# Performance work log

Hardware: AMD Instinct MI355X
Metric: run time of the kernel (lower is better)

The kernel has to match this reference:

```python
import jax, jax.numpy as jnp
import numpy as np

N, E, IN, HID, OUT = 50000, 1600000, 64, 32, 32
NEG_SLOPE = 0.2  # PyG GATConv default


def gat_conv(x, src, dst, W, a_src, a_dst, b, n):
    """Single-head PyG-style GATConv (dropout off / eval mode).
    x: [n, in], src/dst: [E+n] (self-loops already appended),
    W: [in, out], a_src/a_dst: [out], b: [out]."""
    h = x @ W                                   # [n, out]
    e_src = (h * a_src).sum(-1)                 # [n]
    e_dst = (h * a_dst).sum(-1)                 # [n]
    alpha = jax.nn.leaky_relu(e_src[src] + e_dst[dst], NEG_SLOPE)  # [Etot]
    amax = jax.ops.segment_max(alpha, dst, num_segments=n)         # per-dst max
    ex = jnp.exp(alpha - amax[dst])
    denom = jax.ops.segment_sum(ex, dst, num_segments=n)
    coef = ex / denom[dst]                      # softmax over incoming edges
    out = jax.ops.segment_sum(h[src] * coef[:, None], dst, num_segments=n)
    return out + b


def branch(x, src, dst, W1, as1, ad1, b1, W2, as2, ad2, b2, lW, lb, n):
    h = jax.nn.relu(gat_conv(x, src, dst, W1, as1, ad1, b1, n))
    h = jax.nn.relu(gat_conv(h, src, dst, W2, as2, ad2, b2, n))
    return h @ lW + lb


def setup_inputs() -> dict:
    key = jax.random.key(0)
    ks = jax.random.split(key, 32)
    inp = {
        "x": jax.random.normal(ks[0], (N, IN), dtype=jnp.float32),
        "edge_index": jax.random.randint(ks[1], (2, E), 0, N, dtype=jnp.int64),
    }
    i = 2
    for p in ("c", "r"):
        dims = [(IN, HID), (HID, HID)]
        for li, (di, do) in enumerate(dims, start=1):
            s = (2.0 / (di + do)) ** 0.5
            inp[f"{p}_W{li}"] = jax.random.normal(ks[i], (di, do), dtype=jnp.float32) * s; i += 1
            inp[f"{p}_as{li}"] = jax.random.normal(ks[i], (do,), dtype=jnp.float32) * 0.1; i += 1
            inp[f"{p}_ad{li}"] = jax.random.normal(ks[i], (do,), dtype=jnp.float32) * 0.1; i += 1
            inp[f"{p}_b{li}"] = jnp.zeros((do,), dtype=jnp.float32); i += 1
        inp[f"{p}_lW"] = jax.random.normal(ks[i], (HID, OUT), dtype=jnp.float32) * (2.0 / (HID + OUT)) ** 0.5; i += 1
        inp[f"{p}_lb"] = jnp.zeros((OUT,), dtype=jnp.float32); i += 1
    return inp


def reference(x, edge_index,
              c_W1, c_as1, c_ad1, c_b1, c_W2, c_as2, c_ad2, c_b2, c_lW, c_lb,
              r_W1, r_as1, r_ad1, r_b1, r_W2, r_as2, r_ad2, r_b2, r_lW, r_lb):
    n = x.shape[0]
    loop = jnp.arange(n, dtype=edge_index.dtype)
    src = jnp.concatenate([edge_index[0], loop])  # add_self_loops=True default
    dst = jnp.concatenate([edge_index[1], loop])
    prob_zero = jax.nn.sigmoid(branch(x, src, dst, c_W1, c_as1, c_ad1, c_b1,
                                      c_W2, c_as2, c_ad2, c_b2, c_lW, c_lb, n))
    res = branch(x, src, dst, r_W1, r_as1, r_ad1, r_b1,
                 r_W2, r_as2, r_ad2, r_b2, r_lW, r_lb, n)
    return (prob_zero, res)
```

## Files before the change

### kernel.cpp

```cpp
#include <hip/hip_runtime.h>
#include <hip/hip_fp16.h>
#include <math.h>

#define NEG_SLOPE 0.2f

#define DSHIFT 7
#define DSZ 128
#define NBUCK_MAX 512
#define PART_BLOCKS 256

typedef __attribute__((ext_vector_type(8))) _Float16 v8h;
typedef __attribute__((ext_vector_type(4))) float v4f;
typedef __attribute__((ext_vector_type(4))) unsigned int v4u;

__device__ __forceinline__ int ntload_i(const int* p) {
    return __builtin_nontemporal_load(p);
}

__global__ __launch_bounds__(256)
void xcast_kernel(const float* __restrict__ x, _Float16* __restrict__ xh,
                  int total4, int* __restrict__ bcount) {
    int i = blockIdx.x * blockDim.x + threadIdx.x;
    if (i < NBUCK_MAX) bcount[i] = 0;
    if (i >= total4) return;
    float4 v = ((const float4*)x)[i];
    _Float16 o[4] = {(_Float16)v.x, (_Float16)v.y, (_Float16)v.z, (_Float16)v.w};
    ((uint2*)xh)[i] = *(const uint2*)o;
}

__global__ __launch_bounds__(256)
void part_count_kernel(const int* __restrict__ ei, int E, int n, int nbuck,
                       int* __restrict__ bcount) {
    __shared__ int cnt[NBUCK_MAX];
    int t = threadIdx.x;
    for (int k = t; k < nbuck; k += 256) cnt[k] = 0;
    __syncthreads();
    int Etot = E + n;
    int chunk = (Etot + gridDim.x - 1) / gridDim.x;
    int s0 = blockIdx.x * chunk;
    int s1 = min(Etot, s0 + chunk);
    for (int i = s0 + t; i < s1; i += 256) {
        int d = (i < E) ? ntload_i(ei + E + i) : (i - E);
        if ((unsigned)d < (unsigned)n) atomicAdd(&cnt[d >> DSHIFT], 1);
    }
    __syncthreads();
    for (int k = t; k < nbuck; k += 256) {
        int c = cnt[k];
        if (c) atomicAdd(&bcount[k], c);
    }
}

__global__ void bucket_scan_kernel(const int* __restrict__ bcount,
                                   int* __restrict__ colbase,
                                   int* __restrict__ pcur,
                                   int* __restrict__ rptr,
                                   int n, int nbuck) {
    __shared__ int sm[512];
    int t = threadIdx.x;
    int v = (t < nbuck) ? bcount[t] : 0;
    sm[t] = v;
    __syncthreads();
    int x = v;
    for (int off = 1; off < 512; off <<= 1) {
        int y = (t >= off) ? sm[t - off] : 0;
        __syncthreads();
        x += y;
        sm[t] = x;
        __syncthreads();
    }
    if (t < nbuck) { colbase[t] = x - v; pcur[t] = x - v; }
    if (t == nbuck - 1) rptr[n] = x;
}

__global__ __launch_bounds__(256)
void part_write_kernel(const int* __restrict__ ei, int E, int n, int nbuck,
                       int* __restrict__ pcur,
                       unsigned* __restrict__ pairs) {
    __shared__ int cnt[NBUCK_MAX];
    __shared__ int lcur[NBUCK_MAX];
    int t = threadIdx.x;
    for (int k = t; k < nbuck; k += 256) cnt[k] = 0;
    __syncthreads();
    int Etot = E + n;
    int chunk = (Etot + gridDim.x - 1) / gridDim.x;
    int s0 = blockIdx.x * chunk;
    int s1 = min(Etot, s0 + chunk);
    for (int i = s0 + t; i < s1; i += 256) {
        int d = (i < E) ? ntload_i(ei + E + i) : (i - E);
        if ((unsigned)d < (unsigned)n) atomicAdd(&cnt[d >> DSHIFT], 1);
    }
    __syncthreads();
    for (int k = t; k < nbuck; k += 256) {
        int c = cnt[k];
        if (c) lcur[k] = atomicAdd(&pcur[k], c);
    }
    __syncthreads();
    for (int i = s0 + t; i < s1; i += 256) {
        int s, d;
        if (i < E) { s = ntload_i(ei + i); d = ntload_i(ei + E + i); }
        else       { s = d = i - E; }
        if ((unsigned)d < (unsigned)n) {
            if ((unsigned)s >= (unsigned)n) s = 0;
            int pos = atomicAdd(&lcur[d >> DSHIFT], 1);
            pairs[pos] = (unsigned)s | ((unsigned)(d & (DSZ - 1)) << 16);
        }
    }
}

__global__ __launch_bounds__(256)
void fine_kernel(const unsigned* __restrict__ pairs,
                 const int* __restrict__ colbase,
                 const int* __restrict__ bcount,
                 int* __restrict__ rptr,
                 int* __restrict__ col, int n) {
    __shared__ int cnt[DSZ];
    __shared__ int ofs[DSZ];
    int b = blockIdx.x, t = threadIdx.x;
    int p0 = colbase[b], p1 = p0 + bcount[b];
    if (t < DSZ) cnt[t] = 0;
    __syncthreads();
    for (int i = p0 + t; i < p1; i += 256)
        atomicAdd(&cnt[pairs[i] >> 16], 1);
    __syncthreads();
    int v = (t < DSZ) ? cnt[t] : 0;
    if (t < DSZ) ofs[t] = v;
    __syncthreads();
    int x = v;
    for (int off = 1; off < DSZ; off <<= 1) {
        int y = (t >= off && t < DSZ) ? ofs[t - off] : 0;
        __syncthreads();
        if (t < DSZ) { x += y; ofs[t] = x; }
        __syncthreads();
    }
    int d0 = b << DSHIFT;
    if (t < DSZ) {
        int start = p0 + x - v;
        if (d0 + t < n) rptr[d0 + t] = start;
        cnt[t] = start;
    }
    __syncthreads();
    for (int i = p0 + t; i < p1; i += 256) {
        unsigned u = pairs[i];
        int pos = atomicAdd(&cnt[u >> 16], 1);
        col[pos] = (int)(u & 0xFFFFu);
    }
}

__global__ void prep_kernel(const float* __restrict__ cW1, const float* __restrict__ rW1,
                            const float* __restrict__ cas1, const float* __restrict__ cad1,
                            const float* __restrict__ ras1, const float* __restrict__ rad1,
                            const float* __restrict__ cW2, const float* __restrict__ rW2,
                            const float* __restrict__ cas2, const float* __restrict__ cad2,
                            const float* __restrict__ ras2, const float* __restrict__ rad2,
                            const float* __restrict__ clW, const float* __restrict__ rlW,
                            _Float16* __restrict__ WB1,
                            _Float16* __restrict__ WB2,
                            _Float16* __restrict__ WBh) {
    __shared__ float f1s[2][64], f1d[2][64];
    __shared__ float f2s[2][32], f2d[2][32];
    int t = threadIdx.x;
    if (t < 128) {
        int b = t >> 6, k = t & 63;
        const float* W   = b ? rW1 : cW1;
        const float* as_ = b ? ras1 : cas1;
        const float* ad_ = b ? rad1 : cad1;
        float s1 = 0.f, s2 = 0.f;
        for (int f = 0; f < 32; ++f) {
            s1 = fmaf(W[k * 32 + f], as_[f], s1);
            s2 = fmaf(W[k * 32 + f], ad_[f], s2);
        }
        f1s[b][k] = s1;
        f1d[b][k] = s2;
    } else if (t < 192) {
        int b = (t - 128) >> 5, k = (t - 128) & 31;
        const float* W   = b ? rW2 : cW2;
        const float* as_ = b ? ras2 : cas2;
        const float* ad_ = b ? rad2 : cad2;
        float s1 = 0.f, s2 = 0.f;
        for (int f = 0; f < 32; ++f) {
            s1 = fmaf(W[k * 32 + f], as_[f], s1);
            s2 = fmaf(W[k * 32 + f], ad_[f], s2);
        }
        f2s[b][k] = s1;
        f2d[b][k] = s2;
    }
    __syncthreads();
    for (int idx = t; idx < 6144; idx += 256) {
        int blk = idx >> 9;
        int l = (idx >> 3) & 63, j = idx & 7;
        int b = blk / 6, rem = blk % 6, c = rem / 3, tt = rem % 3;
        int k = c * 32 + (l >> 4) * 8 + j;
        int nn = l & 15;
        const float* W = b ? rW1 : cW1;
        float v;
        if (tt < 2) v = W[k * 32 + tt * 16 + nn];
        else v = (nn == 0) ? f1s[b][k] : ((nn == 1) ? f1d[b][k] : 0.f);
        WB1[idx] = (_Float16)v;
    }
    for (int idx = t; idx < 3072; idx += 256) {
        int blk = idx >> 9;
        int l = (idx >> 3) & 63, j = idx & 7;
        int b = blk / 3, tt = blk % 3;
        int k = (l >> 4) * 8 + j;
        int nn = l & 15;
        const float* W = b ? rW2 : cW2;
        float v;
        if (tt < 2) v = W[k * 32 + tt * 16 + nn];
        else v = (nn == 0) ? f2s[b][k] : ((nn == 1) ? f2d[b][k] : 0.f);
        WB2[idx] = (_Float16)v;
    }
    for (int idx = t; idx < 2048; idx += 256) {
        int blk = idx >> 9;
        int l = (idx >> 3) & 63, j = idx & 7;
        int b = blk >> 1, tt = blk & 1;
        int k = (l >> 4) * 8 + j;
        int nn = l & 15;
        const float* W = b ? rlW : clW;
        WBh[idx] = (_Float16)W[k * 32 + tt * 16 + nn];
    }
}

__global__ __launch_bounds__(256)
void t1_mfma_kernel(const _Float16* __restrict__ xh,
                    const _Float16* __restrict__ WB1,
                    _Float16* __restrict__ hC, _Float16* __restrict__ hR,
                    float* __restrict__ esC, float* __restrict__ edC,
                    float* __restrict__ esR, float* __restrict__ edR, int n) {
    int wave = (blockIdx.x * blockDim.x + threadIdx.x) >> 6;
    int lane = threadIdx.x & 63;
    int ntiles = n >> 4;
    if (wave >= ntiles) return;
    int m0 = wave << 4;
    int quad = lane >> 4, nn = lane & 15;
    const _Float16* arow = xh + (size_t)(m0 + nn) * 64 + quad * 8;
    v8h a0 = *(const v8h*)arow;
    v8h a1 = *(const v8h*)(arow + 32);
    v4f acc[2][3];
#pragma unroll
    for (int b = 0; b < 2; ++b)
#pragma unroll
        for (int tt = 0; tt < 3; ++tt) acc[b][tt] = (v4f){0.f, 0.f, 0.f, 0.f};
#pragma unroll
    for (int b = 0; b < 2; ++b) {
#pragma unroll
        for (int c = 0; c < 2; ++c) {
            v8h av = c ? a1 : a0;
#pragma unroll
            for (int tt = 0; tt < 3; ++tt) {
                v8h wb = *(const v8h*)(WB1 + (((b * 2 + c) * 3 + tt) << 9) + lane * 8);
                acc[b][tt] = __builtin_amdgcn_mfma_f32_16x16x32_f16(av, wb, acc[b][tt], 0, 0, 0);
            }
        }
    }
#pragma unroll
    for (int i = 0; i < 4; ++i) {
        int m = m0 + quad * 4 + i;
        size_t r = (size_t)m * 32;
        hC[r + nn]      = (_Float16)acc[0][0][i];
        hC[r + 16 + nn] = (_Float16)acc[0][1][i];
        hR[r + nn]      = (_Float16)acc[1][0][i];
        hR[r + 16 + nn] = (_Float16)acc[1][1][i];
        if (nn == 0) { esC[m] = acc[0][2][i]; esR[m] = acc[1][2][i]; }
        if (nn == 1) { edC[m] = acc[0][2][i]; edR[m] = acc[1][2][i]; }
    }
}

__global__ __launch_bounds__(256)
void t2_mfma_kernel(const _Float16* __restrict__ gC,
                    const _Float16* __restrict__ gR,
                    const _Float16* __restrict__ WB2,
                    _Float16* __restrict__ hC, _Float16* __restrict__ hR,
                    float* __restrict__ esC, float* __restrict__ edC,
                    float* __restrict__ esR, float* __restrict__ edR, int n) {
    int wave = (blockIdx.x * blockDim.x + threadIdx.x) >> 6;
    int lane = threadIdx.x & 63;
    if (wave >= (n >> 4)) return;
    int m0 = wave << 4;
    int quad = lane >> 4, nn = lane & 15;
    v8h aC = *(const v8h*)(gC + (size_t)(m0 + nn) * 32 + quad * 8);
    v8h aR = *(const v8h*)(gR + (size_t)(m0 + nn) * 32 + quad * 8);
    v4f acc[2][3];
#pragma unroll
    for (int b = 0; b < 2; ++b)
#pragma unroll
        for (int tt = 0; tt < 3; ++tt) acc[b][tt] = (v4f){0.f, 0.f, 0.f, 0.f};
#pragma unroll
    for (int b = 0; b < 2; ++b) {
        v8h av = b ? aR : aC;
#pragma unroll
        for (int tt = 0; tt < 3; ++tt) {
            v8h wb = *(const v8h*)(WB2 + ((b * 3 + tt) << 9) + lane * 8);
            acc[b][tt] = __builtin_amdgcn_mfma_f32_16x16x32_f16(av, wb, acc[b][tt], 0, 0, 0);
        }
    }
#pragma unroll
    for (int i = 0; i < 4; ++i) {
        int m = m0 + quad * 4 + i;
        size_t r = (size_t)m * 32;
        hC[r + nn]      = (_Float16)acc[0][0][i];
        hC[r + 16 + nn] = (_Float16)acc[0][1][i];
        hR[r + nn]      = (_Float16)acc[1][0][i];
        hR[r + 16 + nn] = (_Float16)acc[1][1][i];
        if (nn == 0) { esC[m] = acc[0][2][i]; esR[m] = acc[1][2][i]; }
        if (nn == 1) { edC[m] = acc[0][2][i]; edR[m] = acc[1][2][i]; }
    }
}

__global__ __launch_bounds__(256)
void head_mfma_kernel(const _Float16* __restrict__ gC,
                      const _Float16* __restrict__ gR,
                      const _Float16* __restrict__ WBh,
                      const float* __restrict__ clb,
                      const float* __restrict__ rlb,
                      float* __restrict__ out, int n) {
    int wave = (blockIdx.x * blockDim.x + threadIdx.x) >> 6;
    int lane = threadIdx.x & 63;
    if (wave >= (n >> 4)) return;
    int m0 = wave << 4;
    int quad = lane >> 4, nn = lane & 15;
    v8h aC = *(const v8h*)(gC + (size_t)(m0 + nn) * 32 + quad * 8);
    v8h aR = *(const v8h*)(gR + (size_t)(m0 + nn) * 32 + quad * 8);
    v4f acc[2][2];
#pragma unroll
    for (int b = 0; b < 2; ++b)
#pragma unroll
        for (int tt = 0; tt < 2; ++tt) acc[b][tt] = (v4f){0.f, 0.f, 0.f, 0.f};
#pragma unroll
    for (int b = 0; b < 2; ++b) {
        v8h av = b ? aR : aC;
#pragma unroll
        for (int tt = 0; tt < 2; ++tt) {
            v8h wb = *(const v8h*)(WBh + ((b * 2 + tt) << 9) + lane * 8);
            acc[b][tt] = __builtin_amdgcn_mfma_f32_16x16x32_f16(av, wb, acc[b][tt], 0, 0, 0);
        }
    }
    float lb0c = clb[nn], lb1c = clb[16 + nn];
    float lb0r = rlb[nn], lb1r = rlb[16 + nn];
#pragma unroll
    for (int i = 0; i < 4; ++i) {
        int m = m0 + quad * 4 + i;
        float y0 = acc[0][0][i] + lb0c;
        float y1 = acc[0][1][i] + lb1c;
        out[(size_t)m * 32 + nn]      = 1.f / (1.f + __expf(-y0));
        out[(size_t)m * 32 + 16 + nn] = 1.f / (1.f + __expf(-y1));
        out[(size_t)n * 32 + (size_t)m * 32 + nn]      = acc[1][0][i] + lb0r;
        out[(size_t)n * 32 + (size_t)m * 32 + 16 + nn] = acc[1][1][i] + lb1r;
    }
}

__global__ __launch_bounds__(256, 8)
void agg_kernel(const int* __restrict__ rptr,
                const int* __restrict__ col,
                const _Float16* __restrict__ hp,
                const float* __restrict__ es,
                const float* __restrict__ ed,
                const float* __restrict__ bias,
                _Float16* __restrict__ gout, int n) {
    int grp = (blockIdx.x * blockDim.x + threadIdx.x) >> 5;
    int lane = threadIdx.x & 31;
    int sub = lane >> 2;
    int fq  = lane & 3;
    if (grp >= n) return;
    int d = grp;
    int beg = rptr[d], end = rptr[d + 1];
    float edv = ed[d];
    float acc[8];
#pragma unroll
    for (int i = 0; i < 8; ++i) acc[i] = 0.f;
    float l = 0.f;
#pragma unroll 2
    for (int base = beg; base + sub < end; base += 8) {
        int e = base + sub;
        int s = ntload_i(col + e);
        float t = es[s] + edv;
        t = (t > 0.f) ? t : NEG_SLOPE * t;
        float ex = __expf(t);
        l += ex;
        uint4 q = *(const uint4*)(hp + (size_t)s * 32 + fq * 8);
        const __half2* h2 = (const __half2*)&q;
#pragma unroll
        for (int i = 0; i < 4; ++i) {
            float2 v = __half22float2(h2[i]);
            acc[2 * i]     = fmaf(v.x, ex, acc[2 * i]);
            acc[2 * i + 1] = fmaf(v.y, ex, acc[2 * i + 1]);
        }
    }
#pragma unroll
    for (int off = 4; off <= 16; off <<= 1) {
        l += __shfl_xor(l, off, 32);
#pragma unroll
        for (int i = 0; i < 8; ++i) acc[i] += __shfl_xor(acc[i], off, 32);
    }
    if (sub == 0) {
        float il = 1.f / l;
        __half2 o[4];
#pragma unroll
        for (int j = 0; j < 4; ++j) {
            float g0 = fmaxf(acc[2 * j] * il + bias[fq * 8 + 2 * j], 0.f);
            float g1 = fmaxf(acc[2 * j + 1] * il + bias[fq * 8 + 2 * j + 1], 0.f);
            o[j] = __floats2half2_rn(g0, g1);
        }
        __builtin_nontemporal_store(*(const v4u*)o,
                                    (v4u*)(gout + (size_t)d * 32 + fq * 8));
    }
}

extern "C" void kernel_launch(void* const* d_in, const int* in_sizes, int n_in,
                              void* d_out, int out_size, void* d_ws, size_t ws_size,
                              hipStream_t stream) {
    const float* x = (const float*)d_in[0];
    const int* ei = (const int*)d_in[1];
    const int N = in_sizes[0] / 64;
    const int E = in_sizes[1] / 2;
    const int Etot = E + N;

    const float* cW1  = (const float*)d_in[2];
    const float* cas1 = (const float*)d_in[3];
    const float* cad1 = (const float*)d_in[4];
    const float* cb1  = (const float*)d_in[5];
    const float* cW2  = (const float*)d_in[6];
    const float* cas2 = (const float*)d_in[7];
    const float* cad2 = (const float*)d_in[8];
    const float* cb2  = (const float*)d_in[9];
    const float* clW  = (const float*)d_in[10];
    const float* clb  = (const float*)d_in[11];
    const float* rW1  = (const float*)d_in[12];
    const float* ras1 = (const float*)d_in[13];
    const float* rad1 = (const float*)d_in[14];
    const float* rb1  = (const float*)d_in[15];
    const float* rW2  = (const float*)d_in[16];
    const float* ras2 = (const float*)d_in[17];
    const float* rad2 = (const float*)d_in[18];
    const float* rb2  = (const float*)d_in[19];
    const float* rlW  = (const float*)d_in[20];
    const float* rlb  = (const float*)d_in[21];

    const int nbuck = (N + DSZ - 1) >> DSHIFT;

    char* w = (char*)d_ws;
    size_t off = 0;
    auto alloc = [&](size_t bytes) {
        void* p = w + off;
        off = (off + bytes + 255) & ~(size_t)255;
        return p;
    };
    int*       rptr    = (int*)alloc((size_t)(N + 1) * 4);
    int*       bcount  = (int*)alloc(NBUCK_MAX * 4);
    int*       colbase = (int*)alloc(NBUCK_MAX * 4);
    int*       pcur    = (int*)alloc(NBUCK_MAX * 4);
    int*       col     = (int*)alloc((size_t)Etot * 4);
    unsigned*  pairs   = (unsigned*)alloc((size_t)Etot * 4);
    _Float16*  hC      = (_Float16*)alloc((size_t)N * 32 * 2);
    _Float16*  hR      = (_Float16*)alloc((size_t)N * 32 * 2);
    _Float16*  gC      = (_Float16*)alloc((size_t)N * 32 * 2);
    _Float16*  gR      = (_Float16*)alloc((size_t)N * 32 * 2);
    float*     esAC    = (float*)alloc((size_t)N * 4);
    float*     edAC    = (float*)alloc((size_t)N * 4);
    float*     esAR    = (float*)alloc((size_t)N * 4);
    float*     edAR    = (float*)alloc((size_t)N * 4);
    float*     esBC    = (float*)alloc((size_t)N * 4);
    float*     edBC    = (float*)alloc((size_t)N * 4);
    float*     esBR    = (float*)alloc((size_t)N * 4);
    float*     edBR    = (float*)alloc((size_t)N * 4);
    _Float16*  xh      = (_Float16*)alloc((size_t)N * 64 * 2);
    _Float16*  WB1     = (_Float16*)alloc(6144 * 2);
    _Float16*  WB2     = (_Float16*)alloc(3072 * 2);
    _Float16*  WBh     = (_Float16*)alloc(2048 * 2);
    (void)ws_size;

    float* out = (float*)d_out;
    const int node_blocks = (N * 32 + 255) / 256;
    const int xc_blocks   = (N * 64 / 4 + 255) / 256;
    const int mfma_blocks = ((N >> 4) * 64 + 255) / 256;

    xcast_kernel<<<xc_blocks, 256, 0, stream>>>(x, xh, N * 64 / 4, bcount);
    prep_kernel<<<1, 256, 0, stream>>>(cW1, rW1, cas1, cad1, ras1, rad1,
                                       cW2, rW2, cas2, cad2, ras2, rad2,
                                       clW, rlW, WB1, WB2, WBh);
    part_count_kernel<<<PART_BLOCKS, 256, 0, stream>>>(ei, E, N, nbuck, bcount);
    bucket_scan_kernel<<<1, 512, 0, stream>>>(bcount, colbase, pcur, rptr, N, nbuck);
    part_write_kernel<<<PART_BLOCKS, 256, 0, stream>>>(ei, E, N, nbuck, pcur, pairs);
    fine_kernel<<<nbuck, 256, 0, stream>>>(pairs, colbase, bcount, rptr, col, N);

    t1_mfma_kernel<<<mfma_blocks, 256, 0, stream>>>(xh, WB1, hC, hR,
                                                    esAC, edAC, esAR, edAR, N);
    agg_kernel<<<node_blocks, 256, 0, stream>>>(
        rptr, col, hC, esAC, edAC, cb1, gC, N);
    agg_kernel<<<node_blocks, 256, 0, stream>>>(
        rptr, col, hR, esAR, edAR, rb1, gR, N);

    t2_mfma_kernel<<<mfma_blocks, 256, 0, stream>>>(gC, gR, WB2, hC, hR,
                                                    esBC, edBC, esBR, edBR, N);
    agg_kernel<<<node_blocks, 256, 0, stream>>>(
        rptr, col, hC, esBC, edBC, cb2, gC, N);
    agg_kernel<<<node_blocks, 256, 0, stream>>>(
        rptr, col, hR, esBR, edBR, rb2, gR, N);
    head_mfma_kernel<<<mfma_blocks, 256, 0, stream>>>(gC, gR, WBh, clb, rlb, out, N);
}
```

Baseline: 310.5 us.

## Fuse classifier and regressor aggregations and fold x cast into first GEMM

The two per-branch aggregation kernels of each layer are merged into one that walks the CSR neighbour list once and accumulates both branches. The attention scalars are stored interleaved as float2 so one gather serves both branches. The separate fp32→fp16 cast kernel for x is removed: t1 now reads fp32 x and converts in registers, and bucket-count zeroing moves into prep_kernel. This cuts duplicate col/index traffic and launches, at the cost of doubled register pressure in the aggregation kernel, which may lower occupancy.

```diff
diff --git a/kernel.cpp b/kernel.cpp
--- a/kernel.cpp
+++ b/kernel.cpp
@@ -11,21 +11,86 @@
 
 typedef __attribute__((ext_vector_type(8))) _Float16 v8h;
 typedef __attribute__((ext_vector_type(4))) float v4f;
-typedef __attribute__((ext_vector_type(4))) unsigned int v4u;
 
 __device__ __forceinline__ int ntload_i(const int* p) {
     return __builtin_nontemporal_load(p);
 }
 
-__global__ __launch_bounds__(256)
-void xcast_kernel(const float* __restrict__ x, _Float16* __restrict__ xh,
-                  int total4, int* __restrict__ bcount) {
-    int i = blockIdx.x * blockDim.x + threadIdx.x;
-    if (i < NBUCK_MAX) bcount[i] = 0;
-    if (i >= total4) return;
-    float4 v = ((const float4*)x)[i];
-    _Float16 o[4] = {(_Float16)v.x, (_Float16)v.y, (_Float16)v.z, (_Float16)v.w};
-    ((uint2*)xh)[i] = *(const uint2*)o;
+__global__ void prep_kernel(const float* __restrict__ cW1, const float* __restrict__ rW1,
+                            const float* __restrict__ cas1, const float* __restrict__ cad1,
+                            const float* __restrict__ ras1, const float* __restrict__ rad1,
+                            const float* __restrict__ cW2, const float* __restrict__ rW2,
+                            const float* __restrict__ cas2, const float* __restrict__ cad2,
+                            const float* __restrict__ ras2, const float* __restrict__ rad2,
+                            const float* __restrict__ clW, const float* __restrict__ rlW,
+                            _Float16* __restrict__ WB1,
+                            _Float16* __restrict__ WB2,
+                            _Float16* __restrict__ WBh,
+                            int* __restrict__ bcount) {
+    __shared__ float f1s[2][64], f1d[2][64];
+    __shared__ float f2s[2][32], f2d[2][32];
+    int t = threadIdx.x;
+    bcount[t] = 0;
+    bcount[t + 256] = 0;
+    if (t < 128) {
+        int b = t >> 6, k = t & 63;
+        const float* W   = b ? rW1 : cW1;
+        const float* as_ = b ? ras1 : cas1;
+        const float* ad_ = b ? rad1 : cad1;
+        float s1 = 0.f, s2 = 0.f;
+        for (int f = 0; f < 32; ++f) {
+            s1 = fmaf(W[k * 32 + f], as_[f], s1);
+            s2 = fmaf(W[k * 32 + f], ad_[f], s2);
+        }
+        f1s[b][k] = s1;
+        f1d[b][k] = s2;
+    } else if (t < 192) {
+        int b = (t - 128) >> 5, k = (t - 128) & 31;
+        const float* W   = b ? rW2 : cW2;
+        const float* as_ = b ? ras2 : cas2;
+        const float* ad_ = b ? rad2 : cad2;
+        float s1 = 0.f, s2 = 0.f;
+        for (int f = 0; f < 32; ++f) {
+            s1 = fmaf(W[k * 32 + f], as_[f], s1);
+            s2 = fmaf(W[k * 32 + f], ad_[f], s2);
+        }
+        f2s[b][k] = s1;
+        f2d[b][k] = s2;
+    }
+    __syncthreads();
+    for (int idx = t; idx < 6144; idx += 256) {
+        int blk = idx >> 9;
+        int l = (idx >> 3) & 63, j = idx & 7;
+        int b = blk / 6, rem = blk % 6, c = rem / 3, tt = rem % 3;
+        int k = c * 32 + (l >> 4) * 8 + j;
+        int nn = l & 15;
+        const float* W = b ? rW1 : cW1;
+        float v;
+        if (tt < 2) v = W[k * 32 + tt * 16 + nn];
+        else v = (nn == 0) ? f1s[b][k] : ((nn == 1) ? f1d[b][k] : 0.f);
+        WB1[idx] = (_Float16)v;
+    }
+    for (int idx = t; idx < 3072; idx += 256) {
+        int blk = idx >> 9;
+        int l = (idx >> 3) & 63, j = idx & 7;
+        int b = blk / 3, tt = blk % 3;
+        int k = (l >> 4) * 8 + j;
+        int nn = l & 15;
+        const float* W = b ? rW2 : cW2;
+        float v;
+        if (tt < 2) v = W[k * 32 + tt * 16 + nn];
+        else v = (nn == 0) ? f2s[b][k] : ((nn == 1) ? f2d[b][k] : 0.f);
+        WB2[idx] = (_Float16)v;
+    }
+    for (int idx = t; idx < 2048; idx += 256) {
+        int blk = idx >> 9;
+        int l = (idx >> 3) & 63, j = idx & 7;
+        int b = blk >> 1, tt = blk & 1;
+        int k = (l >> 4) * 8 + j;
+        int nn = l & 15;
+        const float* W = b ? rlW : clW;
+        WBh[idx] = (_Float16)W[k * 32 + tt * 16 + nn];
+    }
 }
 
 __global__ __launch_bounds__(256)
@@ -146,95 +211,31 @@
     }
 }
 
-__global__ void prep_kernel(const float* __restrict__ cW1, const float* __restrict__ rW1,
-                            const float* __restrict__ cas1, const float* __restrict__ cad1,
-                            const float* __restrict__ ras1, const float* __restrict__ rad1,
-                            const float* __restrict__ cW2, const float* __restrict__ rW2,
-                            const float* __restrict__ cas2, const float* __restrict__ cad2,
-                            const float* __restrict__ ras2, const float* __restrict__ rad2,
-                            const float* __restrict__ clW, const float* __restrict__ rlW,
-                            _Float16* __restrict__ WB1,
-                            _Float16* __restrict__ WB2,
-                            _Float16* __restrict__ WBh) {
-    __shared__ float f1s[2][64], f1d[2][64];
-    __shared__ float f2s[2][32], f2d[2][32];
-    int t = threadIdx.x;
-    if (t < 128) {
-        int b = t >> 6, k = t & 63;
-        const float* W   = b ? rW1 : cW1;
-        const float* as_ = b ? ras1 : cas1;
-        const float* ad_ = b ? rad1 : cad1;
-        float s1 = 0.f, s2 = 0.f;
-        for (int f = 0; f < 32; ++f) {
-            s1 = fmaf(W[k * 32 + f], as_[f], s1);
-            s2 = fmaf(W[k * 32 + f], ad_[f], s2);
-        }
-        f1s[b][k] = s1;
-        f1d[b][k] = s2;
-    } else if (t < 192) {
-        int b = (t - 128) >> 5, k = (t - 128) & 31;
-        const float* W   = b ? rW2 : cW2;
-        const float* as_ = b ? ras2 : cas2;
-        const float* ad_ = b ? rad2 : cad2;
-        float s1 = 0.f, s2 = 0.f;
-        for (int f = 0; f < 32; ++f) {
-            s1 = fmaf(W[k * 32 + f], as_[f], s1);
-            s2 = fmaf(W[k * 32 + f], ad_[f], s2);
-        }
-        f2s[b][k] = s1;
-        f2d[b][k] = s2;
-    }
-    __syncthreads();
-    for (int idx = t; idx < 6144; idx += 256) {
-        int blk = idx >> 9;
-        int l = (idx >> 3) & 63, j = idx & 7;
-        int b = blk / 6, rem = blk % 6, c = rem / 3, tt = rem % 3;
-        int k = c * 32 + (l >> 4) * 8 + j;
-        int nn = l & 15;
-        const float* W = b ? rW1 : cW1;
-        float v;
-        if (tt < 2) v = W[k * 32 + tt * 16 + nn];
-        else v = (nn == 0) ? f1s[b][k] : ((nn == 1) ? f1d[b][k] : 0.f);
-        WB1[idx] = (_Float16)v;
-    }
-    for (int idx = t; idx < 3072; idx += 256) {
-        int blk = idx >> 9;
-        int l = (idx >> 3) & 63, j = idx & 7;
-        int b = blk / 3, tt = blk % 3;
-        int k = (l >> 4) * 8 + j;
-        int nn = l & 15;
-        const float* W = b ? rW2 : cW2;
-        float v;
-        if (tt < 2) v = W[k * 32 + tt * 16 + nn];
-        else v = (nn == 0) ? f2s[b][k] : ((nn == 1) ? f2d[b][k] : 0.f);
-        WB2[idx] = (_Float16)v;
-    }
-    for (int idx = t; idx < 2048; idx += 256) {
-        int blk = idx >> 9;
-        int l = (idx >> 3) & 63, j = idx & 7;
-        int b = blk >> 1, tt = blk & 1;
-        int k = (l >> 4) * 8 + j;
-        int nn = l & 15;
-        const float* W = b ? rlW : clW;
-        WBh[idx] = (_Float16)W[k * 32 + tt * 16 + nn];
-    }
-}
-
 __global__ __launch_bounds__(256)
-void t1_mfma_kernel(const _Float16* __restrict__ xh,
+void t1_mfma_kernel(const float* __restrict__ x,
                     const _Float16* __restrict__ WB1,
                     _Float16* __restrict__ hC, _Float16* __restrict__ hR,
-                    float* __restrict__ esC, float* __restrict__ edC,
-                    float* __restrict__ esR, float* __restrict__ edR, int n) {
+                    float2* __restrict__ es2, float2* __restrict__ ed2, int n) {
     int wave = (blockIdx.x * blockDim.x + threadIdx.x) >> 6;
     int lane = threadIdx.x & 63;
     int ntiles = n >> 4;
     if (wave >= ntiles) return;
     int m0 = wave << 4;
     int quad = lane >> 4, nn = lane & 15;
-    const _Float16* arow = xh + (size_t)(m0 + nn) * 64 + quad * 8;
-    v8h a0 = *(const v8h*)arow;
-    v8h a1 = *(const v8h*)(arow + 32);
+    const float* xrow = x + (size_t)(m0 + nn) * 64 + quad * 8;
+    float4 f0 = *(const float4*)xrow;
+    float4 f1 = *(const float4*)(xrow + 4);
+    float4 f2 = *(const float4*)(xrow + 32);
+    float4 f3 = *(const float4*)(xrow + 36);
+    v8h a0, a1;
+    a0[0] = (_Float16)f0.x; a0[1] = (_Float16)f0.y;
+    a0[2] = (_Float16)f0.z; a0[3] = (_Float16)f0.w;
+    a0[4] = (_Float16)f1.x; a0[5] = (_Float16)f1.y;
+    a0[6] = (_Float16)f1.z; a0[7] = (_Float16)f1.w;
+    a1[0] = (_Float16)f2.x; a1[1] = (_Float16)f2.y;
+    a1[2] = (_Float16)f2.z; a1[3] = (_Float16)f2.w;
+    a1[4] = (_Float16)f3.x; a1[5] = (_Float16)f3.y;
+    a1[6] = (_Float16)f3.z; a1[7] = (_Float16)f3.w;
     v4f acc[2][3];
 #pragma unroll
     for (int b = 0; b < 2; ++b)
@@ -260,8 +261,8 @@
         hC[r + 16 + nn] = (_Float16)acc[0][1][i];
         hR[r + nn]      = (_Float16)acc[1][0][i];
         hR[r + 16 + nn] = (_Float16)acc[1][1][i];
-        if (nn == 0) { esC[m] = acc[0][2][i]; esR[m] = acc[1][2][i]; }
-        if (nn == 1) { edC[m] = acc[0][2][i]; edR[m] = acc[1][2][i]; }
+        if (nn == 0) es2[m] = make_float2(acc[0][2][i], acc[1][2][i]);
+        if (nn == 1) ed2[m] = make_float2(acc[0][2][i], acc[1][2][i]);
     }
 }
 
@@ -270,8 +271,7 @@
                     const _Float16* __restrict__ gR,
                     const _Float16* __restrict__ WB2,
                     _Float16* __restrict__ hC, _Float16* __restrict__ hR,
-                    float* __restrict__ esC, float* __restrict__ edC,
-                    float* __restrict__ esR, float* __restrict__ edR, int n) {
+                    float2* __restrict__ es2, float2* __restrict__ ed2, int n) {
     int wave = (blockIdx.x * blockDim.x + threadIdx.x) >> 6;
     int lane = threadIdx.x & 63;
     if (wave >= (n >> 4)) return;
@@ -301,8 +301,8 @@
         hC[r + 16 + nn] = (_Float16)acc[0][1][i];
         hR[r + nn]      = (_Float16)acc[1][0][i];
         hR[r + 16 + nn] = (_Float16)acc[1][1][i];
-        if (nn == 0) { esC[m] = acc[0][2][i]; esR[m] = acc[1][2][i]; }
-        if (nn == 1) { edC[m] = acc[0][2][i]; edR[m] = acc[1][2][i]; }
+        if (nn == 0) es2[m] = make_float2(acc[0][2][i], acc[1][2][i]);
+        if (nn == 1) ed2[m] = make_float2(acc[0][2][i], acc[1][2][i]);
     }
 }
 
@@ -351,11 +351,13 @@
 __global__ __launch_bounds__(256, 8)
 void agg_kernel(const int* __restrict__ rptr,
                 const int* __restrict__ col,
-                const _Float16* __restrict__ hp,
-                const float* __restrict__ es,
-                const float* __restrict__ ed,
-                const float* __restrict__ bias,
-                _Float16* __restrict__ gout, int n) {
+                const _Float16* __restrict__ hC,
+                const _Float16* __restrict__ hR,
+                const float2* __restrict__ es2,
+                const float2* __restrict__ ed2,
+                const float* __restrict__ bc,
+                const float* __restrict__ br,
+                _Float16* __restrict__ gC, _Float16* __restrict__ gR, int n) {
     int grp = (blockIdx.x * blockDim.x + threadIdx.x) >> 5;
     int lane = threadIdx.x & 31;
     int sub = lane >> 2;
@@ -363,45 +365,59 @@
     if (grp >= n) return;
     int d = grp;
     int beg = rptr[d], end = rptr[d + 1];
-    float edv = ed[d];
-    float acc[8];
-#pragma unroll
-    for (int i = 0; i < 8; ++i) acc[i] = 0.f;
-    float l = 0.f;
+    float2 edv = ed2[d];
+    float accC[8], accR[8];
+#pragma unroll
+    for (int i = 0; i < 8; ++i) { accC[i] = 0.f; accR[i] = 0.f; }
+    float lc = 0.f, lr = 0.f;
 #pragma unroll 2
     for (int base = beg; base + sub < end; base += 8) {
         int e = base + sub;
         int s = ntload_i(col + e);
-        float t = es[s] + edv;
-        t = (t > 0.f) ? t : NEG_SLOPE * t;
-        float ex = __expf(t);
-        l += ex;
-        uint4 q = *(const uint4*)(hp + (size_t)s * 32 + fq * 8);
-        const __half2* h2 = (const __half2*)&q;
+        float2 ev = es2[s];
+        float tc = ev.x + edv.x, tr = ev.y + edv.y;
+        tc = (tc > 0.f) ? tc : NEG_SLOPE * tc;
+        tr = (tr > 0.f) ? tr : NEG_SLOPE * tr;
+        float exc = __expf(tc), exr = __expf(tr);
+        lc += exc; lr += exr;
+        uint4 qC = *(const uint4*)(hC + (size_t)s * 32 + fq * 8);
+        uint4 qR = *(const uint4*)(hR + (size_t)s * 32 + fq * 8);
+        const __half2* hc2 = (const __half2*)&qC;
+        const __half2* hr2 = (const __half2*)&qR;
 #pragma unroll
         for (int i = 0; i < 4; ++i) {
-            float2 v = __half22float2(h2[i]);
-            acc[2 * i]     = fmaf(v.x, ex, acc[2 * i]);
-            acc[2 * i + 1] = fmaf(v.y, ex, acc[2 * i + 1]);
+            float2 vc = __half22float2(hc2[i]);
+            float2 vr = __half22float2(hr2[i]);
+            accC[2 * i]     = fmaf(vc.x, exc, accC[2 * i]);
+            accC[2 * i + 1] = fmaf(vc.y, exc, accC[2 * i + 1]);
+            accR[2 * i]     = fmaf(vr.x, exr, accR[2 * i]);
+            accR[2 * i + 1] = fmaf(vr.y, exr, accR[2 * i + 1]);
         }
     }
 #pragma unroll
     for (int off = 4; off <= 16; off <<= 1) {
-        l += __shfl_xor(l, off, 32);
-#pragma unroll
-        for (int i = 0; i < 8; ++i) acc[i] += __shfl_xor(acc[i], off, 32);
+        lc += __shfl_xor(lc, off, 32);
+        lr += __shfl_xor(lr, off, 32);
+#pragma unroll
+        for (int i = 0; i < 8; ++i) {
+            accC[i] += __shfl_xor(accC[i], off, 32);
+            accR[i] += __shfl_xor(accR[i], off, 32);
+        }
     }
     if (sub == 0) {
-        float il = 1.f / l;
-        __half2 o[4];
+        float ilc = 1.f / lc, ilr = 1.f / lr;
+        __half2 oc[4], orr[4];
 #pragma unroll
         for (int j = 0; j < 4; ++j) {
-            float g0 = fmaxf(acc[2 * j] * il + bias[fq * 8 + 2 * j], 0.f);
-            float g1 = fmaxf(acc[2 * j + 1] * il + bias[fq * 8 + 2 * j + 1], 0.f);
-            o[j] = __floats2half2_rn(g0, g1);
-        }
-        __builtin_nontemporal_store(*(const v4u*)o,
-                                    (v4u*)(gout + (size_t)d * 32 + fq * 8));
+            float c0 = fmaxf(accC[2 * j] * ilc + bc[fq * 8 + 2 * j], 0.f);
+            float c1 = fmaxf(accC[2 * j + 1] * ilc + bc[fq * 8 + 2 * j + 1], 0.f);
+            float r0 = fmaxf(accR[2 * j] * ilr + br[fq * 8 + 2 * j], 0.f);
+            float r1 = fmaxf(accR[2 * j + 1] * ilr + br[fq * 8 + 2 * j + 1], 0.f);
+            oc[j]  = __floats2half2_rn(c0, c1);
+            orr[j] = __floats2half2_rn(r0, r1);
+        }
+        *(uint4*)(gC + (size_t)d * 32 + fq * 8) = *(const uint4*)oc;
+        *(uint4*)(gR + (size_t)d * 32 + fq * 8) = *(const uint4*)orr;
     }
 }
 
@@ -454,15 +470,10 @@
     _Float16*  hR      = (_Float16*)alloc((size_t)N * 32 * 2);
     _Float16*  gC      = (_Float16*)alloc((size_t)N * 32 * 2);
     _Float16*  gR      = (_Float16*)alloc((size_t)N * 32 * 2);
-    float*     esAC    = (float*)alloc((size_t)N * 4);
-    float*     edAC    = (float*)alloc((size_t)N * 4);
-    float*     esAR    = (float*)alloc((size_t)N * 4);
-    float*     edAR    = (float*)alloc((size_t)N * 4);
-    float*     esBC    = (float*)alloc((size_t)N * 4);
-    float*     edBC    = (float*)alloc((size_t)N * 4);
-    float*     esBR    = (float*)alloc((size_t)N * 4);
-    float*     edBR    = (float*)alloc((size_t)N * 4);
-    _Float16*  xh      = (_Float16*)alloc((size_t)N * 64 * 2);
+    float2*    esA     = (float2*)alloc((size_t)N * 8);
+    float2*    edA     = (float2*)alloc((size_t)N * 8);
+    float2*    esB     = (float2*)alloc((size_t)N * 8);
+    float2*    edB     = (float2*)alloc((size_t)N * 8);
     _Float16*  WB1     = (_Float16*)alloc(6144 * 2);
     _Float16*  WB2     = (_Float16*)alloc(3072 * 2);
     _Float16*  WBh     = (_Float16*)alloc(2048 * 2);
@@ -470,30 +481,22 @@
 
     float* out = (float*)d_out;
     const int node_blocks = (N * 32 + 255) / 256;
-    const int xc_blocks   = (N * 64 / 4 + 255) / 256;
     const int mfma_blocks = ((N >> 4) * 64 + 255) / 256;
 
-    xcast_kernel<<<xc_blocks, 256, 0, stream>>>(x, xh, N * 64 / 4, bcount);
     prep_kernel<<<1, 256, 0, stream>>>(cW1, rW1, cas1, cad1, ras1, rad1,
                                        cW2, rW2, cas2, cad2, ras2, rad2,
-                                       clW, rlW, WB1, WB2, WBh);
+                                       clW, rlW, WB1, WB2, WBh, bcount);
     part_count_kernel<<<PART_BLOCKS, 256, 0, stream>>>(ei, E, N, nbuck, bcount);
     bucket_scan_kernel<<<1, 512, 0, stream>>>(bcount, colbase, pcur, rptr, N, nbuck);
     part_write_kernel<<<PART_BLOCKS, 256, 0, stream>>>(ei, E, N, nbuck, pcur, pairs);
     fine_kernel<<<nbuck, 256, 0, stream>>>(pairs, colbase, bcount, rptr, col, N);
 
-    t1_mfma_kernel<<<mfma_blocks, 256, 0, stream>>>(xh, WB1, hC, hR,
-                                                    esAC, edAC, esAR, edAR, N);
+    t1_mfma_kernel<<<mfma_blocks, 256, 0, stream>>>(x, WB1, hC, hR, esA, edA, N);
     agg_kernel<<<node_blocks, 256, 0, stream>>>(
-        rptr, col, hC, esAC, edAC, cb1, gC, N);
+        rptr, col, hC, hR, esA, edA, cb1, rb1, gC, gR, N);
+
+    t2_mfma_kernel<<<mfma_blocks, 256, 0, stream>>>(gC, gR, WB2, hC, hR, esB, edB, N);
     agg_kernel<<<node_blocks, 256, 0, stream>>>(
-        rptr, col, hR, esAR, edAR, rb1, gR, N);
-
-    t2_mfma_kernel<<<mfma_blocks, 256, 0, stream>>>(gC, gR, WB2, hC, hR,
-                                                    esBC, edBC, esBR, edBR, N);
-    agg_kernel<<<node_blocks, 256, 0, stream>>>(
-        rptr, col, hC, esBC, edBC, cb2, gC, N);
-    agg_kernel<<<node_blocks, 256, 0, stream>>>(
-        rptr, col, hR, esBR, edBR, rb2, gR, N);
+        rptr, col, hC, hR, esB, edB, cb2, rb2, gC, gR, N);
     head_mfma_kernel<<<mfma_blocks, 256, 0, stream>>>(gC, gR, WBh, clb, rlb, out, N);
 }
```

After: 289.7 us. 6.7% less time.
